# Kernel tuning notes

Hardware: AMD Instinct MI355X
Metric: run time of the kernel (lower is better)

## Reference

```python
import jax, jax.numpy as jnp
import numpy as np

INPUT_DIM = 64
HIDDEN_DIM = 512
DIM_INNER = int(HIDDEN_DIM * 1.5)  # 768


def log_g(x):
    # torch.where(x >= 0, (relu(x) + 0.5).log(), -softplus(-x))
    return jnp.where(x >= 0, jnp.log(jax.nn.relu(x) + 0.5), -jax.nn.softplus(-x))


def setup_inputs() -> dict:
    key = jax.random.key(0)
    k_x, k1, k2, k3, k4 = jax.random.split(key, 5)
    B, S = 16, 4096
    x = jax.random.normal(k_x, (B, S, INPUT_DIM), dtype=jnp.float32)
    # weights stored as [in, out] (transpose of torch Linear.weight); bias=False everywhere
    W_in = jax.random.normal(k1, (INPUT_DIM, HIDDEN_DIM), dtype=jnp.float32) * 0.02
    W_hg = jax.random.normal(k2, (HIDDEN_DIM, 2 * DIM_INNER), dtype=jnp.float32) * 0.02
    W_out = jax.random.normal(k3, (DIM_INNER, HIDDEN_DIM), dtype=jnp.float32) * 0.02
    W_final = jax.random.normal(k4, (HIDDEN_DIM, 1), dtype=jnp.float32) * 0.02
    return {"x": x, "W_in": W_in, "W_hg": W_hg, "W_out": W_out, "W_final": W_final}


def reference(x, W_in, W_hg, W_out, W_final):
    # x: [B, S, input_dim]
    h = jnp.einsum('bsi,ih->bsh', x, W_in)                 # [B,S,H]
    hg = jnp.einsum('bsh,hd->bsd', h, W_hg)                # [B,S,2*DI]
    hidden, gate = jnp.split(hg, 2, axis=-1)               # each [B,S,DI]
    # seq_len > 1 path, prev_hidden=None
    log_coeffs = -jax.nn.softplus(gate)                    # log(1 - z)
    log_z = -jax.nn.softplus(-gate)                        # log(z)
    log_values = log_z + log_g(hidden)
    # heinsen associative scan in log space
    a_star = jnp.cumsum(log_coeffs, axis=1)
    log_h = a_star + jax.lax.cumlogsumexp(log_values - a_star, axis=1)
    out = jnp.exp(log_h)                                   # [B,S,DI]
    out = jnp.einsum('bsd,dh->bsh', out, W_out)            # [B,S,H]
    predictions = jnp.einsum('bsh,ho->bso', out, W_final)[..., 0]  # [B,S]
    return predictions
```

## Files before the change

kernel.cpp:

```cpp
#include <hip/hip_runtime.h>
#include <hip/hip_fp16.h>

typedef unsigned short u16;
typedef unsigned int   u32;
typedef __bf16 bf16x8 __attribute__((ext_vector_type(8)));
typedef float  f32x4  __attribute__((ext_vector_type(4)));
typedef float  f32x2  __attribute__((ext_vector_type(2)));

constexpr int BB   = 16;
constexpr int S    = 4096;
constexpr int M    = BB * S;
constexpr int H    = 512;
constexpr int DI   = 768;
constexpr int N2   = 1536;
constexpr int CL   = 128;
constexpr int NCHUNK = M / CL;
constexpr int SEGB  = S / 32;
constexpr int DTILES = 12;
constexpr int NBLK  = NCHUNK * DTILES;

constexpr size_t OFF_B2C   = 0;
constexpr size_t OFF_WC    = 196608;
constexpr size_t OFF_SEGC  = 200704;
constexpr size_t OFF_SEGVH = OFF_SEGC + 6291456;
constexpr size_t OFF_PART  = OFF_SEGVH + 6291456;
constexpr size_t OFF_XB    = OFF_PART + 3145728;

constexpr float L2E = 1.4426950408889634f;

__device__ __forceinline__ u16 f2bf(float f) {
  u32 u = __float_as_uint(f);
  return (u16)((u + 0x7FFFu + ((u >> 16) & 1u)) >> 16);
}

__device__ __forceinline__ u32 pk_bf16(float lo, float hi) {
  u32 r;
  asm("v_cvt_pk_bf16_f32 %0, %1, %2" : "=v"(r) : "v"(lo), "v"(hi));
  return r;
}

__device__ __forceinline__ u32 pk_f16(float lo, float hi) {
  auto p = __builtin_amdgcn_cvt_pkrtz(lo, hi);
  return *(const u32*)&p;
}

__device__ __forceinline__ int cvs(int row, int d) {
  return row * 64 + (d ^ (((row >> 2) & 3) << 4));
}

__device__ __forceinline__ void act_cv2(f32x2 hidden, f32x2 gate,
                                        f32x2& cc, f32x2& vv) {
  f32x2 gs = gate * L2E, hs = hidden * L2E;
  f32x2 eg, eh;
  eg.x = __builtin_amdgcn_exp2f(gs.x);
  eg.y = __builtin_amdgcn_exp2f(gs.y);
  eh.x = __builtin_amdgcn_exp2f(hs.x);
  eh.y = __builtin_amdgcn_exp2f(hs.y);
  f32x2 A = 1.0f + eg, B = 1.0f + eh;
  f32x2 P = A * B;
  f32x2 R;
  R.x = __builtin_amdgcn_rcpf(P.x);
  R.y = __builtin_amdgcn_rcpf(P.y);
  cc = B * R;
  f32x2 hb = (hidden + 0.5f) * B;
  f32x2 w;
  w.x = (hidden.x >= 0.0f) ? hb.x : eh.x;
  w.y = (hidden.y >= 0.0f) ? hb.y : eh.y;
  vv = eg * R * w;
}

__device__ __forceinline__ void comb_step(float& C, float& V, int bit, int ln) {
  float Cp = __shfl_xor(C, bit);
  float Vp = __shfl_xor(V, bit);
  bool up = (ln & bit) != 0;
  V = up ? fmaf(C, Vp, V) : fmaf(Cp, V, Vp);
  C *= Cp;
}

__device__ __forceinline__ void stage_mfma(const u16* __restrict__ xb,
                                           const u16* __restrict__ B2c,
                                           u16* AB, int tid, int m0, int nt,
                                           f32x4 (&acc)[4][4]) {
  const int wv = tid >> 6, ln = tid & 63;
  const int wr = wv >> 1, wcol = wv & 1;
  const int lrow = ln & 15, hi4 = ln >> 4;
  {
    const uint4* gA = (const uint4*)(xb + (size_t)m0 * 64);
    const uint4* gB = (const uint4*)(B2c + (size_t)nt * 128 * 64);
    uint4* lA = (uint4*)AB;
    uint4* lB = (uint4*)(AB + 8192);
    #pragma unroll
    for (int j = 0; j < 4; ++j) {
      int q = j * 256 + tid;
      int qs = (q & ~7) | ((q & 7) ^ ((q >> 3) & 7));
      lA[qs] = gA[q];
      lB[qs] = gB[q];
    }
  }
  __syncthreads();
  {
    const u16* Al = AB;
    const u16* Bl = AB + 8192;
    #pragma unroll
    for (int kk = 0; kk < 2; ++kk) {
      bf16x8 af[4], bfr[4];
      #pragma unroll
      for (int i = 0; i < 4; ++i) {
        int row = wr * 64 + i * 16 + lrow;
        af[i] = *(const bf16x8*)&Al[row * 64 + (((kk * 4 + hi4) ^ (row & 7)) << 3)];
      }
      #pragma unroll
      for (int j = 0; j < 4; ++j) {
        int row = wcol * 64 + j * 16 + lrow;
        bfr[j] = *(const bf16x8*)&Bl[row * 64 + (((kk * 4 + hi4) ^ (row & 7)) << 3)];
      }
      #pragma unroll
      for (int i = 0; i < 4; ++i)
        #pragma unroll
        for (int j = 0; j < 4; ++j)
          acc[i][j] = __builtin_amdgcn_mfma_f32_16x16x32_bf16(af[i], bfr[j], acc[i][j], 0, 0, 0);
    }
  }
}

constexpr int PB_XB = 2048, PB_B2C = 384, PB_WC = 192;
__global__ __launch_bounds__(256) void prep_all(
    const float* __restrict__ x, const float* __restrict__ Win,
    const float* __restrict__ Whg, const float* __restrict__ Wout,
    const float* __restrict__ Wfin,
    u16* __restrict__ xb, u16* __restrict__ B2c, float* __restrict__ wc) {
  __shared__ float Wl[64][65];
  const int tid = threadIdx.x;
  const int bid = blockIdx.x;
  if (bid < PB_XB) {
    size_t i = (size_t)(bid * 256 + tid) * 8;
    float4 f0 = *(const float4*)(x + i);
    float4 f1 = *(const float4*)(x + i + 4);
    uint4 o = make_uint4(pk_bf16(f0.x, f0.y), pk_bf16(f0.z, f0.w),
                         pk_bf16(f1.x, f1.y), pk_bf16(f1.z, f1.w));
    *(uint4*)(xb + i) = o;
  } else if (bid < PB_XB + PB_B2C) {
    const int b = bid - PB_XB;
    const int k = tid & 63;
    const int nloc = tid >> 6;
    const int n = b * 4 + nloc;
    const int g = n >> 5, r = n & 31;
    const int col = (r < 16) ? (g * 16 + r) : (DI + g * 16 + (r - 16));
    float acc = 0.f;
    for (int jc = 0; jc < H; jc += 64) {
      const int jl = tid & 63, k0 = tid >> 6;
      #pragma unroll
      for (int s = 0; s < 16; ++s) {
        int kr = k0 + 4 * s;
        Wl[kr][jl] = Win[kr * H + jc + jl];
      }
      __syncthreads();
      #pragma unroll 8
      for (int j = 0; j < 64; ++j)
        acc = fmaf(Wl[k][j], Whg[(size_t)(jc + j) * N2 + col], acc);
      __syncthreads();
    }
    B2c[n * 64 + k] = f2bf(acc);
  } else {
    const int b = bid - PB_XB - PB_B2C;
    int wv = tid >> 6, ln = tid & 63;
    int d = b * 4 + wv;
    const float* row = Wout + (size_t)d * H;
    float s = 0.f;
    #pragma unroll
    for (int j = 0; j < 8; ++j) {
      int k = j * 64 + ln;
      s += row[k] * Wfin[k];
    }
    #pragma unroll
    for (int off = 32; off; off >>= 1) s += __shfl_xor(s, off);
    if (ln == 0) wc[d] = s;
  }
}

__global__ __launch_bounds__(256) void fused_p1(
    const u16* __restrict__ xb, const u16* __restrict__ B2c,
    float* __restrict__ SegC, float* __restrict__ SegV) {
  __shared__ __align__(16) u16 AB[16384];
  const int tid = threadIdx.x, wv = tid >> 6, ln = tid & 63;
  const int nt = blockIdx.x % DTILES, ck = blockIdx.x / DTILES;
  const int m0 = ck * CL;
  const int wr = wv >> 1, wcol = wv & 1;
  const int lrow = ln & 15, hi4 = ln >> 4;

  f32x4 acc[4][4] = {};
  stage_mfma(xb, B2c, AB, tid, m0, nt, acc);

  #pragma unroll
  for (int jp = 0; jp < 2; ++jp) {
    const int d = nt * 64 + (wcol * 2 + jp) * 16 + lrow;
    #pragma unroll
    for (int sl = 0; sl < 2; ++sl) {
      float Cr[2], Vr[2];
      #pragma unroll
      for (int ii = 0; ii < 2; ++ii) {
        const int i = sl * 2 + ii;
        f32x2 h01 = {acc[i][2 * jp + 0][0], acc[i][2 * jp + 0][1]};
        f32x2 h23 = {acc[i][2 * jp + 0][2], acc[i][2 * jp + 0][3]};
        f32x2 g01 = {acc[i][2 * jp + 1][0], acc[i][2 * jp + 1][1]};
        f32x2 g23 = {acc[i][2 * jp + 1][2], acc[i][2 * jp + 1][3]};
        f32x2 c01, v01, c23, v23;
        act_cv2(h01, g01, c01, v01);
        act_cv2(h23, g23, c23, v23);
        float V = v01.x;
        V = fmaf(c01.y, V, v01.y);
        V = fmaf(c23.x, V, v23.x);
        V = fmaf(c23.y, V, v23.y);
        float C = c01.x * c01.y;
        C *= c23.x;
        C *= c23.y;
        comb_step(C, V, 16, ln);
        comb_step(C, V, 32, ln);
        Cr[ii] = C; Vr[ii] = V;
      }
      float Cs = Cr[0] * Cr[1];
      float Vs = fmaf(Cr[1], Vr[0], Vr[1]);
      if (hi4 == 0) {
        int seg = ck * 4 + wr * 2 + sl;
        SegC[(size_t)seg * DI + d] = Cs;
        SegV[(size_t)seg * DI + d] = Vs;
      }
    }
  }
}

__global__ __launch_bounds__(128) void scan_carry(const float* __restrict__ SegC,
                                                  float* __restrict__ SegVH) {
  const int b = blockIdx.x / 6, dc = blockIdx.x % 6;
  const int d = dc * 128 + threadIdx.x;
  const size_t base = (size_t)b * SEGB * DI + d;
  float carry = 0.f;
  for (int q0 = 0; q0 < SEGB; q0 += 16) {
    float c16[16], v16[16];
    #pragma unroll
    for (int j = 0; j < 16; ++j) {
      size_t idx = base + (size_t)(q0 + j) * DI;
      c16[j] = SegC[idx];
      v16[j] = SegVH[idx];
    }
    #pragma unroll
    for (int j = 0; j < 16; ++j) {
      size_t idx = base + (size_t)(q0 + j) * DI;
      SegVH[idx] = carry;
      carry = fmaf(c16[j], carry, v16[j]);
    }
  }
}

__global__ __launch_bounds__(256) void fused_p2(
    const u16* __restrict__ xb, const u16* __restrict__ B2c,
    const float* __restrict__ Hin, const float* __restrict__ wcomb,
    float* __restrict__ part) {
  __shared__ __align__(16) u16 AB[16384];
  u32* cvl = (u32*)AB;
  const int tid = threadIdx.x, wv = tid >> 6, ln = tid & 63;
  const int nt = blockIdx.x % DTILES, ck = blockIdx.x / DTILES;
  const int m0 = ck * CL;
  const int wr = wv >> 1, wcol = wv & 1;
  const int lrow = ln & 15, hi4 = ln >> 4;

  const int seg = ck * 4 + wv;
  float h = Hin[(size_t)seg * DI + nt * 64 + ln];
  const float wd = wcomb[nt * 64 + ln];

  f32x4 acc[4][4] = {};
  stage_mfma(xb, B2c, AB, tid, m0, nt, acc);
  __syncthreads();

  #pragma unroll
  for (int i = 0; i < 4; ++i)
    #pragma unroll
    for (int jp = 0; jp < 2; ++jp) {
      const int dl = (wcol * 2 + jp) * 16 + lrow;
      const int rb = wr * 64 + i * 16 + hi4 * 4;
      f32x2 h01 = {acc[i][2 * jp + 0][0], acc[i][2 * jp + 0][1]};
      f32x2 h23 = {acc[i][2 * jp + 0][2], acc[i][2 * jp + 0][3]};
      f32x2 g01 = {acc[i][2 * jp + 1][0], acc[i][2 * jp + 1][1]};
      f32x2 g23 = {acc[i][2 * jp + 1][2], acc[i][2 * jp + 1][3]};
      f32x2 c01, v01, c23, v23;
      act_cv2(h01, g01, c01, v01);
      act_cv2(h23, g23, c23, v23);
      cvl[cvs(rb + 0, dl)] = pk_f16(c01.x, v01.x);
      cvl[cvs(rb + 1, dl)] = pk_f16(c01.y, v01.y);
      cvl[cvs(rb + 2, dl)] = pk_f16(c23.x, v23.x);
      cvl[cvs(rb + 3, dl)] = pk_f16(c23.y, v23.y);
    }
  __syncthreads();

  #pragma unroll 4
  for (int tt = 0; tt < 32; ++tt) {
    const int t = wv * 32 + tt;
    u32 u = cvl[cvs(t, ln)];
    float hn;
    asm("v_fma_mix_f32 %0, %1, %2, %1 op_sel:[0,0,1] op_sel_hi:[1,0,1]"
        : "=v"(hn) : "v"(u), "v"(h));
    h = hn;
    float pv = h * wd;
    cvl[t * 64 + ((ln + t) & 63)] = __float_as_uint(pv);
  }
  __syncthreads();
  const int row = tid >> 1, half = tid & 1;
  float s = 0.f;
  #pragma unroll 8
  for (int jj = 0; jj < 32; ++jj) {
    int idx = (half * 32 + jj + row) & 63;
    s += __uint_as_float(cvl[row * 64 + idx]);
  }
  s += __shfl_xor(s, 1);
  if (half == 0) part[(size_t)nt * M + m0 + row] = s;
}

__global__ __launch_bounds__(256) void reduce12(const float* __restrict__ part,
                                                float* __restrict__ out) {
  int i = blockIdx.x * 256 + threadIdx.x;
  float s = 0.f;
  #pragma unroll
  for (int w = 0; w < DTILES; ++w) s += part[(size_t)w * M + i];
  out[i] = s;
}

extern "C" void kernel_launch(void* const* d_in, const int* in_sizes, int n_in,
                              void* d_out, int out_size, void* d_ws, size_t ws_size,
                              hipStream_t stream) {
  const float* x    = (const float*)d_in[0];
  const float* Win  = (const float*)d_in[1];
  const float* Whg  = (const float*)d_in[2];
  const float* Wout = (const float*)d_in[3];
  const float* Wfin = (const float*)d_in[4];
  float* out = (float*)d_out;
  char* ws = (char*)d_ws;

  u16*   B2c   = (u16*)(ws + OFF_B2C);
  float* wc    = (float*)(ws + OFF_WC);
  float* SegC  = (float*)(ws + OFF_SEGC);
  float* SegVH = (float*)(ws + OFF_SEGVH);
  float* part  = (float*)(ws + OFF_PART);
  u16*   xb    = (u16*)(ws + OFF_XB);

  prep_all  <<<PB_XB + PB_B2C + PB_WC, 256, 0, stream>>>(x, Win, Whg, Wout, Wfin,
                                                          xb, B2c, wc);
  fused_p1  <<<NBLK, 256, 0, stream>>>(xb, B2c, SegC, SegVH);
  scan_carry<<<96, 128, 0, stream>>>(SegC, SegVH);
  fused_p2  <<<NBLK, 256, 0, stream>>>(xb, B2c, SegVH, wc, part);
  reduce12  <<<256, 256, 0, stream>>>(part, out);
}
```

Before: 131.3 us.

## Fuse chunked scan into a persistent per-batch chain kernel

Replaces the two-pass design with one persistent kernel. Previously the first pass computed segment summaries, a separate kernel scanned the carries, and a second pass recomputed the GEMM. Now each block owns one (batch, d-tile) pair and walks all sequence chunks in order, carrying the hidden state in shared memory. This removes the duplicated projection GEMM, the segment-summary global traffic and one launch. It also prefetches the next chunk's input into registers. The cost is much less parallelism (192 blocks, one per CU) and a serial dependency across 32 chunk iterations, each with several block-wide barriers, so latency hiding is weaker.

```diff
diff --git a/kernel.cpp b/kernel.cpp
--- a/kernel.cpp
+++ b/kernel.cpp
@@ -14,17 +14,14 @@
 constexpr int DI   = 768;
 constexpr int N2   = 1536;
 constexpr int CL   = 128;
-constexpr int NCHUNK = M / CL;
-constexpr int SEGB  = S / 32;
+constexpr int NT   = S / CL;
 constexpr int DTILES = 12;
-constexpr int NBLK  = NCHUNK * DTILES;
-
-constexpr size_t OFF_B2C   = 0;
-constexpr size_t OFF_WC    = 196608;
-constexpr size_t OFF_SEGC  = 200704;
-constexpr size_t OFF_SEGVH = OFF_SEGC + 6291456;
-constexpr size_t OFF_PART  = OFF_SEGVH + 6291456;
-constexpr size_t OFF_XB    = OFF_PART + 3145728;
+constexpr int NCHAIN = BB * DTILES;
+
+constexpr size_t OFF_B2C  = 0;
+constexpr size_t OFF_WC   = 196608;
+constexpr size_t OFF_PART = 200704;
+constexpr size_t OFF_XB   = OFF_PART + 3145728;
 
 constexpr float L2E = 1.4426950408889634f;
 
@@ -75,52 +72,6 @@
   bool up = (ln & bit) != 0;
   V = up ? fmaf(C, Vp, V) : fmaf(Cp, V, Vp);
   C *= Cp;
-}
-
-__device__ __forceinline__ void stage_mfma(const u16* __restrict__ xb,
-                                           const u16* __restrict__ B2c,
-                                           u16* AB, int tid, int m0, int nt,
-                                           f32x4 (&acc)[4][4]) {
-  const int wv = tid >> 6, ln = tid & 63;
-  const int wr = wv >> 1, wcol = wv & 1;
-  const int lrow = ln & 15, hi4 = ln >> 4;
-  {
-    const uint4* gA = (const uint4*)(xb + (size_t)m0 * 64);
-    const uint4* gB = (const uint4*)(B2c + (size_t)nt * 128 * 64);
-    uint4* lA = (uint4*)AB;
-    uint4* lB = (uint4*)(AB + 8192);
-    #pragma unroll
-    for (int j = 0; j < 4; ++j) {
-      int q = j * 256 + tid;
-      int qs = (q & ~7) | ((q & 7) ^ ((q >> 3) & 7));
-      lA[qs] = gA[q];
-      lB[qs] = gB[q];
-    }
-  }
-  __syncthreads();
-  {
-    const u16* Al = AB;
-    const u16* Bl = AB + 8192;
-    #pragma unroll
-    for (int kk = 0; kk < 2; ++kk) {
-      bf16x8 af[4], bfr[4];
-      #pragma unroll
-      for (int i = 0; i < 4; ++i) {
-        int row = wr * 64 + i * 16 + lrow;
-        af[i] = *(const bf16x8*)&Al[row * 64 + (((kk * 4 + hi4) ^ (row & 7)) << 3)];
-      }
-      #pragma unroll
-      for (int j = 0; j < 4; ++j) {
-        int row = wcol * 64 + j * 16 + lrow;
-        bfr[j] = *(const bf16x8*)&Bl[row * 64 + (((kk * 4 + hi4) ^ (row & 7)) << 3)];
-      }
-      #pragma unroll
-      for (int i = 0; i < 4; ++i)
-        #pragma unroll
-        for (int j = 0; j < 4; ++j)
-          acc[i][j] = __builtin_amdgcn_mfma_f32_16x16x32_bf16(af[i], bfr[j], acc[i][j], 0, 0, 0);
-    }
-  }
 }
 
 constexpr int PB_XB = 2048, PB_B2C = 384, PB_WC = 192;
@@ -178,141 +129,165 @@
   }
 }
 
-__global__ __launch_bounds__(256) void fused_p1(
+__global__ __launch_bounds__(256, 1) void fused_chain(
     const u16* __restrict__ xb, const u16* __restrict__ B2c,
-    float* __restrict__ SegC, float* __restrict__ SegV) {
-  __shared__ __align__(16) u16 AB[16384];
+    const float* __restrict__ wcomb, float* __restrict__ part) {
+  __shared__ __align__(16) u16 Al[8192];
+  __shared__ __align__(16) u16 Bl[8192];
+  __shared__ __align__(16) u32 cvl[8192];
+  __shared__ float SCs[4][64], SVs[4][64];
+  __shared__ float Hl[64];
+
   const int tid = threadIdx.x, wv = tid >> 6, ln = tid & 63;
-  const int nt = blockIdx.x % DTILES, ck = blockIdx.x / DTILES;
-  const int m0 = ck * CL;
+  const int b = blockIdx.x & 15, nt = blockIdx.x >> 4;
   const int wr = wv >> 1, wcol = wv & 1;
   const int lrow = ln & 15, hi4 = ln >> 4;
-
-  f32x4 acc[4][4] = {};
-  stage_mfma(xb, B2c, AB, tid, m0, nt, acc);
-
+  const float wd = wcomb[nt * 64 + ln];
+
+  {
+    const uint4* gB = (const uint4*)(B2c + (size_t)nt * 128 * 64);
+    uint4* lB = (uint4*)Bl;
+    #pragma unroll
+    for (int j = 0; j < 4; ++j) {
+      int q = j * 256 + tid;
+      int qs = (q & ~7) | ((q & 7) ^ ((q >> 3) & 7));
+      lB[qs] = gB[q];
+    }
+  }
+  const uint4* gA = (const uint4*)(xb + (size_t)b * S * 64);
+  uint4 aw[4];
   #pragma unroll
-  for (int jp = 0; jp < 2; ++jp) {
-    const int d = nt * 64 + (wcol * 2 + jp) * 16 + lrow;
-    #pragma unroll
-    for (int sl = 0; sl < 2; ++sl) {
-      float Cr[2], Vr[2];
-      #pragma unroll
-      for (int ii = 0; ii < 2; ++ii) {
-        const int i = sl * 2 + ii;
-        f32x2 h01 = {acc[i][2 * jp + 0][0], acc[i][2 * jp + 0][1]};
-        f32x2 h23 = {acc[i][2 * jp + 0][2], acc[i][2 * jp + 0][3]};
-        f32x2 g01 = {acc[i][2 * jp + 1][0], acc[i][2 * jp + 1][1]};
-        f32x2 g23 = {acc[i][2 * jp + 1][2], acc[i][2 * jp + 1][3]};
-        f32x2 c01, v01, c23, v23;
-        act_cv2(h01, g01, c01, v01);
-        act_cv2(h23, g23, c23, v23);
-        float V = v01.x;
-        V = fmaf(c01.y, V, v01.y);
-        V = fmaf(c23.x, V, v23.x);
-        V = fmaf(c23.y, V, v23.y);
-        float C = c01.x * c01.y;
-        C *= c23.x;
-        C *= c23.y;
-        comb_step(C, V, 16, ln);
-        comb_step(C, V, 32, ln);
-        Cr[ii] = C; Vr[ii] = V;
-      }
-      float Cs = Cr[0] * Cr[1];
-      float Vs = fmaf(Cr[1], Vr[0], Vr[1]);
-      if (hi4 == 0) {
-        int seg = ck * 4 + wr * 2 + sl;
-        SegC[(size_t)seg * DI + d] = Cs;
-        SegV[(size_t)seg * DI + d] = Vs;
-      }
+  for (int j = 0; j < 4; ++j) aw[j] = gA[j * 256 + tid];
+  {
+    uint4* lA = (uint4*)Al;
+    #pragma unroll
+    for (int j = 0; j < 4; ++j) {
+      int q = j * 256 + tid;
+      int qs = (q & ~7) | ((q & 7) ^ ((q >> 3) & 7));
+      lA[qs] = aw[j];
     }
   }
-}
-
-__global__ __launch_bounds__(128) void scan_carry(const float* __restrict__ SegC,
-                                                  float* __restrict__ SegVH) {
-  const int b = blockIdx.x / 6, dc = blockIdx.x % 6;
-  const int d = dc * 128 + threadIdx.x;
-  const size_t base = (size_t)b * SEGB * DI + d;
-  float carry = 0.f;
-  for (int q0 = 0; q0 < SEGB; q0 += 16) {
-    float c16[16], v16[16];
-    #pragma unroll
-    for (int j = 0; j < 16; ++j) {
-      size_t idx = base + (size_t)(q0 + j) * DI;
-      c16[j] = SegC[idx];
-      v16[j] = SegVH[idx];
-    }
-    #pragma unroll
-    for (int j = 0; j < 16; ++j) {
-      size_t idx = base + (size_t)(q0 + j) * DI;
-      SegVH[idx] = carry;
-      carry = fmaf(c16[j], carry, v16[j]);
-    }
-  }
-}
-
-__global__ __launch_bounds__(256) void fused_p2(
-    const u16* __restrict__ xb, const u16* __restrict__ B2c,
-    const float* __restrict__ Hin, const float* __restrict__ wcomb,
-    float* __restrict__ part) {
-  __shared__ __align__(16) u16 AB[16384];
-  u32* cvl = (u32*)AB;
-  const int tid = threadIdx.x, wv = tid >> 6, ln = tid & 63;
-  const int nt = blockIdx.x % DTILES, ck = blockIdx.x / DTILES;
-  const int m0 = ck * CL;
-  const int wr = wv >> 1, wcol = wv & 1;
-  const int lrow = ln & 15, hi4 = ln >> 4;
-
-  const int seg = ck * 4 + wv;
-  float h = Hin[(size_t)seg * DI + nt * 64 + ln];
-  const float wd = wcomb[nt * 64 + ln];
-
-  f32x4 acc[4][4] = {};
-  stage_mfma(xb, B2c, AB, tid, m0, nt, acc);
-  __syncthreads();
-
-  #pragma unroll
-  for (int i = 0; i < 4; ++i)
+  if (tid < 64) Hl[tid] = 0.f;
+
+  for (int t = 0; t < NT; ++t) {
+    __syncthreads();
+
+    f32x4 acc[4][4] = {};
+    #pragma unroll
+    for (int kk = 0; kk < 2; ++kk) {
+      bf16x8 af[4], bfr[4];
+      #pragma unroll
+      for (int i = 0; i < 4; ++i) {
+        int row = wr * 64 + i * 16 + lrow;
+        af[i] = *(const bf16x8*)&Al[row * 64 + (((kk * 4 + hi4) ^ (row & 7)) << 3)];
+      }
+      #pragma unroll
+      for (int j = 0; j < 4; ++j) {
+        int row = wcol * 64 + j * 16 + lrow;
+        bfr[j] = *(const bf16x8*)&Bl[row * 64 + (((kk * 4 + hi4) ^ (row & 7)) << 3)];
+      }
+      #pragma unroll
+      for (int i = 0; i < 4; ++i)
+        #pragma unroll
+        for (int j = 0; j < 4; ++j)
+          acc[i][j] = __builtin_amdgcn_mfma_f32_16x16x32_bf16(af[i], bfr[j], acc[i][j], 0, 0, 0);
+    }
+
+    if (t < NT - 1) {
+      #pragma unroll
+      for (int j = 0; j < 4; ++j) aw[j] = gA[(t + 1) * 1024 + j * 256 + tid];
+    }
+
+    u32 cvp[2][4][4];
     #pragma unroll
     for (int jp = 0; jp < 2; ++jp) {
       const int dl = (wcol * 2 + jp) * 16 + lrow;
-      const int rb = wr * 64 + i * 16 + hi4 * 4;
-      f32x2 h01 = {acc[i][2 * jp + 0][0], acc[i][2 * jp + 0][1]};
-      f32x2 h23 = {acc[i][2 * jp + 0][2], acc[i][2 * jp + 0][3]};
-      f32x2 g01 = {acc[i][2 * jp + 1][0], acc[i][2 * jp + 1][1]};
-      f32x2 g23 = {acc[i][2 * jp + 1][2], acc[i][2 * jp + 1][3]};
-      f32x2 c01, v01, c23, v23;
-      act_cv2(h01, g01, c01, v01);
-      act_cv2(h23, g23, c23, v23);
-      cvl[cvs(rb + 0, dl)] = pk_f16(c01.x, v01.x);
-      cvl[cvs(rb + 1, dl)] = pk_f16(c01.y, v01.y);
-      cvl[cvs(rb + 2, dl)] = pk_f16(c23.x, v23.x);
-      cvl[cvs(rb + 3, dl)] = pk_f16(c23.y, v23.y);
-    }
-  __syncthreads();
-
-  #pragma unroll 4
-  for (int tt = 0; tt < 32; ++tt) {
-    const int t = wv * 32 + tt;
-    u32 u = cvl[cvs(t, ln)];
-    float hn;
-    asm("v_fma_mix_f32 %0, %1, %2, %1 op_sel:[0,0,1] op_sel_hi:[1,0,1]"
-        : "=v"(hn) : "v"(u), "v"(h));
-    h = hn;
-    float pv = h * wd;
-    cvl[t * 64 + ((ln + t) & 63)] = __float_as_uint(pv);
+      #pragma unroll
+      for (int sl = 0; sl < 2; ++sl) {
+        float Cr[2], Vr[2];
+        #pragma unroll
+        for (int ii = 0; ii < 2; ++ii) {
+          const int i = sl * 2 + ii;
+          f32x2 h01 = {acc[i][2 * jp + 0][0], acc[i][2 * jp + 0][1]};
+          f32x2 h23 = {acc[i][2 * jp + 0][2], acc[i][2 * jp + 0][3]};
+          f32x2 g01 = {acc[i][2 * jp + 1][0], acc[i][2 * jp + 1][1]};
+          f32x2 g23 = {acc[i][2 * jp + 1][2], acc[i][2 * jp + 1][3]};
+          f32x2 c01, v01, c23, v23;
+          act_cv2(h01, g01, c01, v01);
+          act_cv2(h23, g23, c23, v23);
+          cvp[jp][i][0] = pk_f16(c01.x, v01.x);
+          cvp[jp][i][1] = pk_f16(c01.y, v01.y);
+          cvp[jp][i][2] = pk_f16(c23.x, v23.x);
+          cvp[jp][i][3] = pk_f16(c23.y, v23.y);
+          float V = v01.x;
+          V = fmaf(c01.y, V, v01.y);
+          V = fmaf(c23.x, V, v23.x);
+          V = fmaf(c23.y, V, v23.y);
+          float C = c01.x * c01.y;
+          C *= c23.x;
+          C *= c23.y;
+          comb_step(C, V, 16, ln);
+          comb_step(C, V, 32, ln);
+          Cr[ii] = C; Vr[ii] = V;
+        }
+        float Cs = Cr[0] * Cr[1];
+        float Vs = fmaf(Cr[1], Vr[0], Vr[1]);
+        if (hi4 == 0) {
+          SCs[wr * 2 + sl][dl] = Cs;
+          SVs[wr * 2 + sl][dl] = Vs;
+        }
+      }
+    }
+    __syncthreads();
+
+    if (t < NT - 1) {
+      uint4* lA = (uint4*)Al;
+      #pragma unroll
+      for (int j = 0; j < 4; ++j) {
+        int q = j * 256 + tid;
+        int qs = (q & ~7) | ((q & 7) ^ ((q >> 3) & 7));
+        lA[qs] = aw[j];
+      }
+    }
+    #pragma unroll
+    for (int jp = 0; jp < 2; ++jp) {
+      const int dl = (wcol * 2 + jp) * 16 + lrow;
+      #pragma unroll
+      for (int i = 0; i < 4; ++i)
+        #pragma unroll
+        for (int r = 0; r < 4; ++r)
+          cvl[cvs(wr * 64 + i * 16 + hi4 * 4 + r, dl)] = cvp[jp][i][r];
+    }
+    float h = Hl[ln];
+    if (wv >= 1) h = fmaf(SCs[0][ln], h, SVs[0][ln]);
+    if (wv >= 2) h = fmaf(SCs[1][ln], h, SVs[1][ln]);
+    if (wv >= 3) h = fmaf(SCs[2][ln], h, SVs[2][ln]);
+    __syncthreads();
+
+    #pragma unroll 4
+    for (int tt = 0; tt < 32; ++tt) {
+      const int lr = wv * 32 + tt;
+      u32 u = cvl[cvs(lr, ln)];
+      float hn;
+      asm("v_fma_mix_f32 %0, %1, %2, %1 op_sel:[0,0,1] op_sel_hi:[1,0,1]"
+          : "=v"(hn) : "v"(u), "v"(h));
+      h = hn;
+      float pv = h * wd;
+      cvl[lr * 64 + ((ln + lr) & 63)] = __float_as_uint(pv);
+    }
+    if (wv == 3) Hl[ln] = h;
+    __syncthreads();
+
+    const int row = tid >> 1, half = tid & 1;
+    float s = 0.f;
+    #pragma unroll 8
+    for (int jj = 0; jj < 32; ++jj) {
+      int idx = (half * 32 + jj + row) & 63;
+      s += __uint_as_float(cvl[row * 64 + idx]);
+    }
+    s += __shfl_xor(s, 1);
+    if (half == 0) part[(size_t)nt * M + (size_t)b * S + t * CL + row] = s;
   }
-  __syncthreads();
-  const int row = tid >> 1, half = tid & 1;
-  float s = 0.f;
-  #pragma unroll 8
-  for (int jj = 0; jj < 32; ++jj) {
-    int idx = (half * 32 + jj + row) & 63;
-    s += __uint_as_float(cvl[row * 64 + idx]);
-  }
-  s += __shfl_xor(s, 1);
-  if (half == 0) part[(size_t)nt * M + m0 + row] = s;
 }
 
 __global__ __launch_bounds__(256) void reduce12(const float* __restrict__ part,
@@ -335,17 +310,13 @@
   float* out = (float*)d_out;
   char* ws = (char*)d_ws;
 
-  u16*   B2c   = (u16*)(ws + OFF_B2C);
-  float* wc    = (float*)(ws + OFF_WC);
-  float* SegC  = (float*)(ws + OFF_SEGC);
-  float* SegVH = (float*)(ws + OFF_SEGVH);
-  float* part  = (float*)(ws + OFF_PART);
-  u16*   xb    = (u16*)(ws + OFF_XB);
-
-  prep_all  <<<PB_XB + PB_B2C + PB_WC, 256, 0, stream>>>(x, Win, Whg, Wout, Wfin,
-                                                          xb, B2c, wc);
-  fused_p1  <<<NBLK, 256, 0, stream>>>(xb, B2c, SegC, SegVH);
-  scan_carry<<<96, 128, 0, stream>>>(SegC, SegVH);
-  fused_p2  <<<NBLK, 256, 0, stream>>>(xb, B2c, SegVH, wc, part);
-  reduce12  <<<256, 256, 0, stream>>>(part, out);
-}
+  u16*   B2c  = (u16*)(ws + OFF_B2C);
+  float* wc   = (float*)(ws + OFF_WC);
+  float* part = (float*)(ws + OFF_PART);
+  u16*   xb   = (u16*)(ws + OFF_XB);
+
+  prep_all   <<<PB_XB + PB_B2C + PB_WC, 256, 0, stream>>>(x, Win, Whg, Wout, Wfin,
+                                                           xb, B2c, wc);
+  fused_chain<<<NCHAIN, 256, 0, stream>>>(xb, B2c, wc, part);
+  reduce12   <<<256, 256, 0, stream>>>(part, out);
+}
```

Result: slower. 196.8 us (+49.9%).

## Transpose LDS scan tile to d-major for 128-bit accesses and replace shuffle combine

Applied to the files above, without the earlier changes.

In the second pass, the per-row (c,v) tile in shared memory becomes d-major with an XOR swizzle. Each lane can then write and read four consecutive timesteps as one 128-bit access during the sequential scan, and the final row reduction indexes the transposed layout. In the first pass, the cross-lane shuffle combine is replaced by writing per-quad partials to a padded shared array and combining them serially per segment after a barrier. This cuts the count of LDS instructions and shuffles, at the cost of an extra shared buffer and a barrier in the first pass.

```diff
diff --git a/kernel.cpp b/kernel.cpp
--- a/kernel.cpp
+++ b/kernel.cpp
@@ -44,8 +44,8 @@
   return *(const u32*)&p;
 }
 
-__device__ __forceinline__ int cvs(int row, int d) {
-  return row * 64 + (d ^ (((row >> 2) & 3) << 4));
+__device__ __forceinline__ int cvtx(int d, int rowq) {
+  return d * 128 + (rowq ^ ((d & 7) << 2));
 }
 
 __device__ __forceinline__ void act_cv2(f32x2 hidden, f32x2 gate,
@@ -67,14 +67,6 @@
   w.x = (hidden.x >= 0.0f) ? hb.x : eh.x;
   w.y = (hidden.y >= 0.0f) ? hb.y : eh.y;
   vv = eg * R * w;
-}
-
-__device__ __forceinline__ void comb_step(float& C, float& V, int bit, int ln) {
-  float Cp = __shfl_xor(C, bit);
-  float Vp = __shfl_xor(V, bit);
-  bool up = (ln & bit) != 0;
-  V = up ? fmaf(C, Vp, V) : fmaf(Cp, V, Vp);
-  C *= Cp;
 }
 
 __device__ __forceinline__ void stage_mfma(const u16* __restrict__ xb,
@@ -182,6 +174,7 @@
     const u16* __restrict__ xb, const u16* __restrict__ B2c,
     float* __restrict__ SegC, float* __restrict__ SegV) {
   __shared__ __align__(16) u16 AB[16384];
+  __shared__ float runC[32][65], runV[32][65];
   const int tid = threadIdx.x, wv = tid >> 6, ln = tid & 63;
   const int nt = blockIdx.x % DTILES, ck = blockIdx.x / DTILES;
   const int m0 = ck * CL;
@@ -193,40 +186,41 @@
 
   #pragma unroll
   for (int jp = 0; jp < 2; ++jp) {
-    const int d = nt * 64 + (wcol * 2 + jp) * 16 + lrow;
-    #pragma unroll
-    for (int sl = 0; sl < 2; ++sl) {
-      float Cr[2], Vr[2];
-      #pragma unroll
-      for (int ii = 0; ii < 2; ++ii) {
-        const int i = sl * 2 + ii;
-        f32x2 h01 = {acc[i][2 * jp + 0][0], acc[i][2 * jp + 0][1]};
-        f32x2 h23 = {acc[i][2 * jp + 0][2], acc[i][2 * jp + 0][3]};
-        f32x2 g01 = {acc[i][2 * jp + 1][0], acc[i][2 * jp + 1][1]};
-        f32x2 g23 = {acc[i][2 * jp + 1][2], acc[i][2 * jp + 1][3]};
-        f32x2 c01, v01, c23, v23;
-        act_cv2(h01, g01, c01, v01);
-        act_cv2(h23, g23, c23, v23);
-        float V = v01.x;
-        V = fmaf(c01.y, V, v01.y);
-        V = fmaf(c23.x, V, v23.x);
-        V = fmaf(c23.y, V, v23.y);
-        float C = c01.x * c01.y;
-        C *= c23.x;
-        C *= c23.y;
-        comb_step(C, V, 16, ln);
-        comb_step(C, V, 32, ln);
-        Cr[ii] = C; Vr[ii] = V;
-      }
-      float Cs = Cr[0] * Cr[1];
-      float Vs = fmaf(Cr[1], Vr[0], Vr[1]);
-      if (hi4 == 0) {
-        int seg = ck * 4 + wr * 2 + sl;
-        SegC[(size_t)seg * DI + d] = Cs;
-        SegV[(size_t)seg * DI + d] = Vs;
-      }
-    }
-  }
+    const int dl = (wcol * 2 + jp) * 16 + lrow;
+    #pragma unroll
+    for (int i = 0; i < 4; ++i) {
+      f32x2 h01 = {acc[i][2 * jp + 0][0], acc[i][2 * jp + 0][1]};
+      f32x2 h23 = {acc[i][2 * jp + 0][2], acc[i][2 * jp + 0][3]};
+      f32x2 g01 = {acc[i][2 * jp + 1][0], acc[i][2 * jp + 1][1]};
+      f32x2 g23 = {acc[i][2 * jp + 1][2], acc[i][2 * jp + 1][3]};
+      f32x2 c01, v01, c23, v23;
+      act_cv2(h01, g01, c01, v01);
+      act_cv2(h23, g23, c23, v23);
+      float V = v01.x;
+      V = fmaf(c01.y, V, v01.y);
+      V = fmaf(c23.x, V, v23.x);
+      V = fmaf(c23.y, V, v23.y);
+      float C = c01.x * c01.y;
+      C *= c23.x;
+      C *= c23.y;
+      const int q = wr * 16 + i * 4 + hi4;
+      runC[q][dl] = C;
+      runV[q][dl] = V;
+    }
+  }
+  __syncthreads();
+
+  float C = runC[wv * 8][ln], V = runV[wv * 8][ln];
+  #pragma unroll
+  for (int q8 = 1; q8 < 8; ++q8) {
+    float rc = runC[wv * 8 + q8][ln];
+    float rv = runV[wv * 8 + q8][ln];
+    V = fmaf(rc, V, rv);
+    C *= rc;
+  }
+  const int seg = ck * 4 + wv;
+  SegC[(size_t)seg * DI + nt * 64 + ln] = C;
+  SegV[(size_t)seg * DI + nt * 64 + ln] = V;
 }
 
 __global__ __launch_bounds__(128) void scan_carry(const float* __restrict__ SegC,
@@ -257,7 +251,7 @@
     const float* __restrict__ Hin, const float* __restrict__ wcomb,
     float* __restrict__ part) {
   __shared__ __align__(16) u16 AB[16384];
-  u32* cvl = (u32*)AB;
+  u32* cvt = (u32*)AB;
   const int tid = threadIdx.x, wv = tid >> 6, ln = tid & 63;
   const int nt = blockIdx.x % DTILES, ck = blockIdx.x / DTILES;
   const int m0 = ck * CL;
@@ -273,11 +267,10 @@
   __syncthreads();
 
   #pragma unroll
-  for (int i = 0; i < 4; ++i)
-    #pragma unroll
-    for (int jp = 0; jp < 2; ++jp) {
-      const int dl = (wcol * 2 + jp) * 16 + lrow;
-      const int rb = wr * 64 + i * 16 + hi4 * 4;
+  for (int jp = 0; jp < 2; ++jp) {
+    const int dl = (wcol * 2 + jp) * 16 + lrow;
+    #pragma unroll
+    for (int i = 0; i < 4; ++i) {
       f32x2 h01 = {acc[i][2 * jp + 0][0], acc[i][2 * jp + 0][1]};
       f32x2 h23 = {acc[i][2 * jp + 0][2], acc[i][2 * jp + 0][3]};
       f32x2 g01 = {acc[i][2 * jp + 1][0], acc[i][2 * jp + 1][1]};
@@ -285,31 +278,43 @@
       f32x2 c01, v01, c23, v23;
       act_cv2(h01, g01, c01, v01);
       act_cv2(h23, g23, c23, v23);
-      cvl[cvs(rb + 0, dl)] = pk_f16(c01.x, v01.x);
-      cvl[cvs(rb + 1, dl)] = pk_f16(c01.y, v01.y);
-      cvl[cvs(rb + 2, dl)] = pk_f16(c23.x, v23.x);
-      cvl[cvs(rb + 3, dl)] = pk_f16(c23.y, v23.y);
-    }
-  __syncthreads();
-
-  #pragma unroll 4
-  for (int tt = 0; tt < 32; ++tt) {
-    const int t = wv * 32 + tt;
-    u32 u = cvl[cvs(t, ln)];
+      const int rb = wr * 64 + i * 16 + hi4 * 4;
+      uint4 qd = make_uint4(pk_f16(c01.x, v01.x), pk_f16(c01.y, v01.y),
+                            pk_f16(c23.x, v23.x), pk_f16(c23.y, v23.y));
+      *(uint4*)&cvt[cvtx(dl, rb)] = qd;
+    }
+  }
+  __syncthreads();
+
+  #pragma unroll
+  for (int tq = 0; tq < 8; ++tq) {
+    const int t4 = wv * 32 + tq * 4;
+    u32* slot = &cvt[cvtx(ln, t4)];
+    uint4 q = *(const uint4*)slot;
     float hn;
+    uint4 pv;
     asm("v_fma_mix_f32 %0, %1, %2, %1 op_sel:[0,0,1] op_sel_hi:[1,0,1]"
-        : "=v"(hn) : "v"(u), "v"(h));
-    h = hn;
-    float pv = h * wd;
-    cvl[t * 64 + ((ln + t) & 63)] = __float_as_uint(pv);
-  }
-  __syncthreads();
+        : "=v"(hn) : "v"(q.x), "v"(h));
+    h = hn; pv.x = __float_as_uint(h * wd);
+    asm("v_fma_mix_f32 %0, %1, %2, %1 op_sel:[0,0,1] op_sel_hi:[1,0,1]"
+        : "=v"(hn) : "v"(q.y), "v"(h));
+    h = hn; pv.y = __float_as_uint(h * wd);
+    asm("v_fma_mix_f32 %0, %1, %2, %1 op_sel:[0,0,1] op_sel_hi:[1,0,1]"
+        : "=v"(hn) : "v"(q.z), "v"(h));
+    h = hn; pv.z = __float_as_uint(h * wd);
+    asm("v_fma_mix_f32 %0, %1, %2, %1 op_sel:[0,0,1] op_sel_hi:[1,0,1]"
+        : "=v"(hn) : "v"(q.w), "v"(h));
+    h = hn; pv.w = __float_as_uint(h * wd);
+    *(uint4*)slot = pv;
+  }
+  __syncthreads();
+
   const int row = tid >> 1, half = tid & 1;
   float s = 0.f;
   #pragma unroll 8
   for (int jj = 0; jj < 32; ++jj) {
-    int idx = (half * 32 + jj + row) & 63;
-    s += __uint_as_float(cvl[row * 64 + idx]);
+    int d = half * 32 + ((jj + row) & 31);
+    s += __uint_as_float(cvt[d * 128 + ((row & ~3) ^ ((d & 7) << 2)) + (row & 3)]);
   }
   s += __shfl_xor(s, 1);
   if (half == 0) part[(size_t)nt * M + m0 + row] = s;
```

Result: faster. 126.9 us (-3.4%).
